# Kernel optimization log

Measured on AMD Instinct MI355X. Metric: run time of the kernel, lower is better.

## Reference

```python
import jax, jax.numpy as jnp
import numpy as np

B, S, H = 2, 2048, 2048
N_HEADS, N_KV, HEAD_DIM = 16, 8, 128
EPS = 1e-6
ROPE_THETA = 1e6


def _rms_norm(x, w, eps=EPS):
    # per-head RMSNorm over last dim (head_dim), computed in fp32
    xf = x.astype(jnp.float32)
    var = jnp.mean(xf * xf, axis=-1, keepdims=True)
    return (w * (xf * jax.lax.rsqrt(var + eps))).astype(x.dtype)


def _rotate_half(x):
    x1, x2 = jnp.split(x, 2, axis=-1)
    return jnp.concatenate((-x2, x1), axis=-1)


def setup_inputs() -> dict:
    key = jax.random.key(0)
    ks = jax.random.split(key, 6)
    hidden_states = jax.random.normal(ks[0], (B, S, H), dtype=jnp.float32)
    # RoPE tables: [B, S, head_dim]
    inv_freq = 1.0 / (ROPE_THETA ** (np.arange(0, HEAD_DIM, 2, dtype=np.float32) / HEAD_DIM))
    pos = np.arange(S, dtype=np.float32)
    freqs = np.outer(pos, inv_freq)                      # [S, head_dim/2]
    emb = np.concatenate([freqs, freqs], axis=-1)        # [S, head_dim]
    cos = jnp.broadcast_to(jnp.asarray(np.cos(emb)), (B, S, HEAD_DIM))
    sin = jnp.broadcast_to(jnp.asarray(np.sin(emb)), (B, S, HEAD_DIM))
    # additive causal mask [B, 1, S, S]
    causal = jnp.triu(jnp.full((S, S), -1e9, dtype=jnp.float32), k=1)
    attention_mask = jnp.broadcast_to(causal[None, None], (B, 1, S, S))
    scale = 0.02
    Wq = jax.random.normal(ks[1], (N_HEADS * HEAD_DIM, H), dtype=jnp.float32) * scale
    Wk = jax.random.normal(ks[2], (N_KV * HEAD_DIM, H), dtype=jnp.float32) * scale
    Wv = jax.random.normal(ks[3], (N_KV * HEAD_DIM, H), dtype=jnp.float32) * scale
    Wo = jax.random.normal(ks[4], (H, N_HEADS * HEAD_DIM), dtype=jnp.float32) * scale
    q_norm_w = jnp.ones((HEAD_DIM,), dtype=jnp.float32)
    k_norm_w = jnp.ones((HEAD_DIM,), dtype=jnp.float32)
    return dict(hidden_states=hidden_states, cos=cos, sin=sin,
                attention_mask=attention_mask, Wq=Wq, Wk=Wk, Wv=Wv, Wo=Wo,
                q_norm_w=q_norm_w, k_norm_w=k_norm_w)


def reference(hidden_states, cos, sin, attention_mask, Wq, Wk, Wv, Wo, q_norm_w, k_norm_w):
    b, s, _ = hidden_states.shape
    scaling = HEAD_DIM ** -0.5
    n_rep = N_HEADS // N_KV
    # QKV projections (torch Linear: x @ W.T), split into heads
    q = jnp.einsum('bsh,dh->bsd', hidden_states, Wq).reshape(b, s, N_HEADS, HEAD_DIM)
    k = jnp.einsum('bsh,dh->bsd', hidden_states, Wk).reshape(b, s, N_KV, HEAD_DIM)
    v = jnp.einsum('bsh,dh->bsd', hidden_states, Wv).reshape(b, s, N_KV, HEAD_DIM)
    # per-head QK RMSNorm, then [B, H, S, D]
    q = _rms_norm(q, q_norm_w).transpose(0, 2, 1, 3)
    k = _rms_norm(k, k_norm_w).transpose(0, 2, 1, 3)
    v = v.transpose(0, 2, 1, 3)
    # RoPE (cos/sin unsqueezed over head dim)
    c = cos[:, None, :, :]
    sn = sin[:, None, :, :]
    q = q * c + _rotate_half(q) * sn
    k = k * c + _rotate_half(k) * sn
    # GQA: repeat kv heads
    k = jnp.repeat(k, n_rep, axis=1)
    v = jnp.repeat(v, n_rep, axis=1)
    # eager attention: materialize full [B, H, S, S] scores
    attn_weights = jnp.einsum('bhqd,bhkd->bhqk', q, k) * scaling + attention_mask
    attn_weights = jax.nn.softmax(attn_weights.astype(jnp.float32), axis=-1).astype(q.dtype)
    attn_output = jnp.einsum('bhqk,bhkd->bhqd', attn_weights, v)
    attn_output = attn_output.transpose(0, 2, 1, 3).reshape(b, s, N_HEADS * HEAD_DIM)
    attn_output = jnp.einsum('bsd,hd->bsh', attn_output, Wo)
    return attn_output, attn_weights
```

## Files before the change

### kernel.cpp

```cpp
#include <hip/hip_runtime.h>
#include <stdint.h>

typedef unsigned short u16;
typedef __attribute__((ext_vector_type(8))) short bf16x8;
typedef __attribute__((ext_vector_type(4))) float f32x4;
typedef __attribute__((ext_vector_type(4))) unsigned short u16x4;
typedef __attribute__((ext_vector_type(8))) unsigned short u16x8;

#define SCALE_LOG2E 0.12751743007633614f

__device__ __forceinline__ u16 f2bf(float x){
  uint32_t u = __float_as_uint(x);
  u += 0x7FFFu + ((u >> 16) & 1u);
  return (u16)(u >> 16);
}
__device__ __forceinline__ float bf2f(u16 h){
  return __uint_as_float(((uint32_t)h) << 16);
}
__device__ __forceinline__ void gload16(const void* g, void* l){
  __builtin_amdgcn_global_load_lds((const __attribute__((address_space(1))) void*)g,
                                   (__attribute__((address_space(3))) void*)l, 16, 0, 0);
}

__global__ __launch_bounds__(256) void k_cvt5(
    const float* __restrict__ s0, u16* __restrict__ d0,
    const float* __restrict__ s1, u16* __restrict__ d1,
    const float* __restrict__ s2, u16* __restrict__ d2,
    const float* __restrict__ s3, u16* __restrict__ d3,
    const float* __restrict__ s4, u16* __restrict__ d4)
{
  int b = blockIdx.x;
  const float* s; u16* d; int off;
  if      (b < 8192)  { s=s0; d=d0; off=b; }
  else if (b < 12288) { s=s1; d=d1; off=b-8192; }
  else if (b < 14336) { s=s2; d=d2; off=b-12288; }
  else if (b < 16384) { s=s3; d=d3; off=b-14336; }
  else                { s=s4; d=d4; off=b-16384; }
  size_t i = ((size_t)off * 256 + threadIdx.x) * 4;
  float4 v = *(const float4*)(s + i);
  ushort4 o;
  o.x = f2bf(v.x); o.y = f2bf(v.y); o.z = f2bf(v.z); o.w = f2bf(v.w);
  *(ushort4*)(d + i) = o;
}

#define STAGE_UNIT(PTR, ROWOFF, BUF, TENS, KS, T1) do{ \
  _Pragma("unroll") \
  for(int jj=0;jj<2;jj++){ \
    int rs_ = wid*32 + jj*16 + (lane>>2); \
    int kp_ = (lane&3) ^ ((rs_>>1)&3); \
    gload16((PTR) + (size_t)((ROWOFF)+rs_)*K + (size_t)(T1)*64 + (KS)*32 + kp_*8, \
            &lds[BUF][TENS][KS][(wid*2+jj)*512]); \
  }}while(0)

#define FRAG(BASE, ROW) (*(const bf16x8*)((BASE) + (ROW)*32 + ((c_ ^ (((ROW)>>1)&3))<<3)))

__global__ __launch_bounds__(512,2) void k_gemm256(
    const u16* __restrict__ A, const u16* __restrict__ Bw, void* __restrict__ Cout,
    int N, int K, int ldc, int out_f32)
{
  __shared__ u16 lds[2][2][2][256*32];
  const int tid = threadIdx.x, wid = tid>>6, lane = tid&63;
  const int nbn = N >> 8;
  const int cpx = gridDim.x >> 3;
  const int bid = (blockIdx.x & 7)*cpx + (blockIdx.x >> 3);
  const int bm = bid / nbn, bn = bid % nbn;
  const int m0 = bm<<8, n0 = bn<<8;
  const int wm = wid>>2, wn = wid&3;
  const int c_ = lane>>4, rl = lane&15;

  f32x4 acc[8][4];
  f32x4 zero4 = {0.f,0.f,0.f,0.f};
#pragma unroll
  for (int i=0;i<8;i++)
#pragma unroll
    for (int j=0;j<4;j++) acc[i][j] = zero4;

  STAGE_UNIT(A,  m0, 0, 0, 0, 0);
  STAGE_UNIT(Bw, n0, 0, 1, 0, 0);
  STAGE_UNIT(A,  m0, 0, 0, 1, 0);
  STAGE_UNIT(Bw, n0, 0, 1, 1, 0);

  const int nt = K >> 6;
#pragma unroll 2
  for (int t=0; t<nt; ++t) {
    const int cur = t&1, nxt = cur^1;
    const bool pf = (t+1 < nt);
    const u16* Ab0 = lds[cur][0][0];
    const u16* Bb0 = lds[cur][1][0];
    const u16* Ab1 = lds[cur][0][1];
    const u16* Bb1 = lds[cur][1][1];
    bf16x8 af[4], bf[4];

    asm volatile("s_waitcnt vmcnt(4)" ::: "memory");
    __builtin_amdgcn_s_barrier();
    asm volatile("" ::: "memory");
#pragma unroll
    for (int j=0;j<4;j++) bf[j] = FRAG(Bb0, wn*64 + j*16 + rl);
#pragma unroll
    for (int i=0;i<4;i++) af[i] = FRAG(Ab0, wm*128 + i*16 + rl);
    if (pf) STAGE_UNIT(A, m0, nxt, 0, 0, t+1);
    __builtin_amdgcn_s_setprio(1);
#pragma unroll
    for (int i=0;i<4;i++)
#pragma unroll
      for (int j=0;j<4;j++)
        acc[i][j] = __builtin_amdgcn_mfma_f32_16x16x32_bf16(af[i], bf[j], acc[i][j], 0,0,0);
    __builtin_amdgcn_s_setprio(0);
    __builtin_amdgcn_s_barrier();
    asm volatile("" ::: "memory");

#pragma unroll
    for (int i=0;i<4;i++) af[i] = FRAG(Ab0, wm*128 + (i+4)*16 + rl);
    if (pf) STAGE_UNIT(Bw, n0, nxt, 1, 0, t+1);
    __builtin_amdgcn_s_setprio(1);
#pragma unroll
    for (int i=0;i<4;i++)
#pragma unroll
      for (int j=0;j<4;j++)
        acc[i+4][j] = __builtin_amdgcn_mfma_f32_16x16x32_bf16(af[i], bf[j], acc[i+4][j], 0,0,0);
    __builtin_amdgcn_s_setprio(0);
    __builtin_amdgcn_s_barrier();
    asm volatile("" ::: "memory");

    if (pf) { asm volatile("s_waitcnt vmcnt(4)" ::: "memory"); }
    else    { asm volatile("s_waitcnt vmcnt(0)" ::: "memory"); }
    __builtin_amdgcn_s_barrier();
    asm volatile("" ::: "memory");
#pragma unroll
    for (int j=0;j<4;j++) bf[j] = FRAG(Bb1, wn*64 + j*16 + rl);
#pragma unroll
    for (int i=0;i<4;i++) af[i] = FRAG(Ab1, wm*128 + i*16 + rl);
    if (pf) STAGE_UNIT(A, m0, nxt, 0, 1, t+1);
    __builtin_amdgcn_s_setprio(1);
#pragma unroll
    for (int i=0;i<4;i++)
#pragma unroll
      for (int j=0;j<4;j++)
        acc[i][j] = __builtin_amdgcn_mfma_f32_16x16x32_bf16(af[i], bf[j], acc[i][j], 0,0,0);
    __builtin_amdgcn_s_setprio(0);
    __builtin_amdgcn_s_barrier();
    asm volatile("" ::: "memory");

#pragma unroll
    for (int i=0;i<4;i++) af[i] = FRAG(Ab1, wm*128 + (i+4)*16 + rl);
    if (pf) STAGE_UNIT(Bw, n0, nxt, 1, 1, t+1);
    __builtin_amdgcn_s_setprio(1);
#pragma unroll
    for (int i=0;i<4;i++)
#pragma unroll
      for (int j=0;j<4;j++)
        acc[i+4][j] = __builtin_amdgcn_mfma_f32_16x16x32_bf16(af[i], bf[j], acc[i+4][j], 0,0,0);
    __builtin_amdgcn_s_setprio(0);
    __builtin_amdgcn_s_barrier();
    asm volatile("" ::: "memory");
  }

  const int r0 = m0 + wm*128 + ((lane>>4)<<2);
  const int c0 = n0 + wn*64 + rl;
  if (out_f32) {
    float* C = (float*)Cout;
#pragma unroll
    for (int i=0;i<8;i++)
#pragma unroll
      for (int j=0;j<4;j++)
#pragma unroll
        for (int r=0;r<4;r++)
          C[(size_t)(r0 + i*16 + r)*ldc + (c0 + j*16)] = acc[i][j][r];
  } else {
    u16* C = (u16*)Cout;
#pragma unroll
    for (int i=0;i<8;i++)
#pragma unroll
      for (int j=0;j<4;j++)
#pragma unroll
        for (int r=0;r<4;r++)
          C[(size_t)(r0 + i*16 + r)*ldc + (c0 + j*16)] = f2bf(acc[i][j][r]);
  }
}

#define STAGE_A128(BUF, KS, T1) do{ \
  int rs_ = wid*16 + (lane>>2); \
  int kp_ = (lane&3) ^ ((rs_>>1)&3); \
  gload16(A + (size_t)(m0+rs_)*K + (size_t)(T1)*64 + (KS)*32 + kp_*8, \
          &ldsA[BUF][KS][wid*512]); \
  }while(0)

#define STAGE_B128(BUF, KS, T1) do{ \
  _Pragma("unroll") \
  for(int jj=0;jj<2;jj++){ \
    int rs_ = wid*32 + jj*16 + (lane>>2); \
    int kp_ = (lane&3) ^ ((rs_>>1)&3); \
    gload16(Bw + (size_t)(n0+rs_)*K + (size_t)(T1)*64 + (KS)*32 + kp_*8, \
            &ldsB[BUF][KS][(wid*2+jj)*512]); \
  }}while(0)

__global__ __launch_bounds__(512,2) void k_gemm_bm128(
    const u16* __restrict__ A, const u16* __restrict__ Bw, float* __restrict__ C,
    int N, int K, int ldc)
{
  __shared__ u16 ldsA[2][2][128*32];
  __shared__ u16 ldsB[2][2][256*32];
  const int tid = threadIdx.x, wid = tid>>6, lane = tid&63;
  const int nbn = N >> 8;
  const int cpx = gridDim.x >> 3;
  const int bid = (blockIdx.x & 7)*cpx + (blockIdx.x >> 3);
  const int bm = bid / nbn, bn = bid % nbn;
  const int m0 = bm<<7, n0 = bn<<8;
  const int wm = wid>>2, wn = wid&3;
  const int c_ = lane>>4, rl = lane&15;

  f32x4 acc[4][4];
  f32x4 zero4 = {0.f,0.f,0.f,0.f};
#pragma unroll
  for (int i=0;i<4;i++)
#pragma unroll
    for (int j=0;j<4;j++) acc[i][j] = zero4;

  STAGE_A128(0, 0, 0);
  STAGE_B128(0, 0, 0);
  STAGE_A128(0, 1, 0);
  STAGE_B128(0, 1, 0);

  const int nt = K >> 6;
#pragma unroll 2
  for (int t=0; t<nt; ++t) {
    const int cur = t&1, nxt = cur^1;
    const bool pf = (t+1 < nt);
    bf16x8 af[4], bf[4];

    asm volatile("s_waitcnt vmcnt(3)" ::: "memory");
    __builtin_amdgcn_s_barrier();
    asm volatile("" ::: "memory");
#pragma unroll
    for (int i=0;i<4;i++) af[i] = FRAG(ldsA[cur][0], wm*64 + i*16 + rl);
#pragma unroll
    for (int j=0;j<4;j++) bf[j] = FRAG(ldsB[cur][0], wn*64 + j*16 + rl);
    if (pf) { STAGE_A128(nxt, 0, t+1); STAGE_B128(nxt, 0, t+1); }
    __builtin_amdgcn_s_setprio(1);
#pragma unroll
    for (int i=0;i<4;i++)
#pragma unroll
      for (int j=0;j<4;j++)
        acc[i][j] = __builtin_amdgcn_mfma_f32_16x16x32_bf16(af[i], bf[j], acc[i][j], 0,0,0);
    __builtin_amdgcn_s_setprio(0);
    __builtin_amdgcn_s_barrier();
    asm volatile("" ::: "memory");

    if (pf) { asm volatile("s_waitcnt vmcnt(3)" ::: "memory"); }
    else    { asm volatile("s_waitcnt vmcnt(0)" ::: "memory"); }
    __builtin_amdgcn_s_barrier();
    asm volatile("" ::: "memory");
#pragma unroll
    for (int i=0;i<4;i++) af[i] = FRAG(ldsA[cur][1], wm*64 + i*16 + rl);
#pragma unroll
    for (int j=0;j<4;j++) bf[j] = FRAG(ldsB[cur][1], wn*64 + j*16 + rl);
    if (pf) { STAGE_A128(nxt, 1, t+1); STAGE_B128(nxt, 1, t+1); }
    __builtin_amdgcn_s_setprio(1);
#pragma unroll
    for (int i=0;i<4;i++)
#pragma unroll
      for (int j=0;j<4;j++)
        acc[i][j] = __builtin_amdgcn_mfma_f32_16x16x32_bf16(af[i], bf[j], acc[i][j], 0,0,0);
    __builtin_amdgcn_s_setprio(0);
    __builtin_amdgcn_s_barrier();
    asm volatile("" ::: "memory");
  }

  const int r0 = m0 + wm*64 + ((lane>>4)<<2);
  const int c0 = n0 + wn*64 + rl;
#pragma unroll
  for (int i=0;i<4;i++)
#pragma unroll
    for (int j=0;j<4;j++)
#pragma unroll
      for (int r=0;r<4;r++)
        C[(size_t)(r0 + i*16 + r)*ldc + (c0 + j*16)] = acc[i][j][r];
}

__global__ __launch_bounds__(256) void k_normrope(
    u16* __restrict__ qkv, const float* __restrict__ cosb, const float* __restrict__ sinb,
    const float* __restrict__ qw, const float* __restrict__ kw)
{
  const int tid = threadIdx.x, lane = tid&63;
  const int task = blockIdx.x*4 + (tid>>6);
  int bs, col; const float* w;
  if (task < 65536) { bs = task >> 4; col = (task & 15)*128; w = qw; }
  else { int t2 = task - 65536; bs = t2 >> 3; col = 2048 + (t2 & 7)*128; w = kw; }
  u16* row = qkv + (size_t)bs*4096 + col;
  float x0 = bf2f(row[lane]), x1 = bf2f(row[lane+64]);
  float ss = x0*x0 + x1*x1;
#pragma unroll
  for (int m=1; m<64; m<<=1) ss += __shfl_xor(ss, m, 64);
  float rn = rsqrtf(ss*(1.0f/128.0f) + 1e-6f);
  const float* cp = cosb + (size_t)bs*128;
  const float* sp = sinb + (size_t)bs*128;
  float q0 = x0*rn*w[lane], q1 = x1*rn*w[lane+64];
  float o0 = q0*cp[lane]    - q1*sp[lane];
  float o1 = q1*cp[lane+64] + q0*sp[lane+64];
  row[lane]    = f2bf(o0);
  row[lane+64] = f2bf(o1);
}

__global__ __launch_bounds__(256) void k_vtrans(const u16* __restrict__ qkv, u16* __restrict__ vt)
{
  const int bid = blockIdx.x;
  const int dt = bid & 1, st = (bid>>1)&31, kvh = (bid>>6)&7, b = bid>>9;
  __shared__ u16 tile[64][72];
  const int tid = threadIdx.x;
  const int rr = tid >> 3, c = (tid & 7) * 8;
  const u16* src = qkv + ((size_t)(b*2048 + st*64))*4096 + 3072 + kvh*128 + dt*64;
#pragma unroll
  for (int p=0;p<2;p++){
    int sl = p*32 + rr;
    u16x8 v = *(const u16x8*)(src + (size_t)sl*4096 + c);
#pragma unroll
    for (int e=0;e<8;e++) tile[sl][c+e] = v[e];
  }
  __syncthreads();
  u16* dst = vt + ((size_t)((b*8+kvh)*128 + dt*64))*2048 + st*64;
#pragma unroll
  for (int p=0;p<2;p++){
    int dl = p*32 + rr;
    u16x8 o;
#pragma unroll
    for (int e=0;e<8;e++) o[e] = tile[c+e][dl];
    *(u16x8*)(dst + (size_t)dl*2048 + c) = o;
  }
}

#define STAGE_K(T, DSTBUF) do { \
  _Pragma("unroll") \
  for (int i_=0;i_<4;i_++){ \
    int r_ = wv*16 + i_*4 + (lane>>4); \
    int cs_ = (lane&15) ^ (r_&7); \
    gload16(Kb + (size_t)((T)*64 + r_)*4096 + cs_*8, (DSTBUF) + (wv*4+i_)*512); \
  } } while(0)

#define STAGE_V(T, DSTBUF) do { \
  _Pragma("unroll") \
  for (int i_=0;i_<4;i_++){ \
    int d_ = wv*32 + i_*8 + (lane>>3); \
    int cs_ = (lane&7) ^ (d_&7); \
    gload16(Vb + (size_t)d_*2048 + (T)*64 + cs_*8, (DSTBUF) + (wv*4+i_)*512); \
  } } while(0)

#define COMPUTE_S16(SACC, KBUF) do { \
  _Pragma("unroll") \
  for (int ks_=0;ks_<4;ks_++){ \
    bf16x8 bfr_[4]; \
    _Pragma("unroll") \
    for (int ns_=0;ns_<4;ns_++){ \
      int n_ = ns_*16 + (lane&15); \
      int sl_ = (ks_*4 + (lane>>4)) ^ (n_&7); \
      bfr_[ns_] = *(const bf16x8*)((KBUF) + n_*128 + sl_*8); \
    } \
    _Pragma("unroll") \
    for (int ns_=0;ns_<4;ns_++) \
      SACC[ns_] = __builtin_amdgcn_mfma_f32_16x16x32_bf16(qf[ks_], bfr_[ns_], SACC[ns_], 0,0,0); \
  } } while(0)

__global__ __launch_bounds__(256) void k_lsum(
    const u16* __restrict__ qkv, float* __restrict__ lsum)
{
  __shared__ u16 lK[2][64*128];
  const int tid = threadIdx.x, wv = tid>>6, lane = tid&63;
  const int rl = lane&15, hi = lane>>4;
  const int bh = blockIdx.x & 31;
  const int h = bh & 15, b = bh >> 4;
  const int seg = blockIdx.x >> 5;
  const int kvh = h>>1;
  const u16* Qb = qkv + (size_t)b*2048*4096 + h*128;
  const u16* Kb = qkv + (size_t)b*2048*4096 + 2048 + kvh*128;
  float* lrow = lsum + (size_t)bh*2048;

  f32x4 zero4 = {0.f,0.f,0.f,0.f};
  int jj[8], kk[8];
#pragma unroll
  for (int i=0;i<8;i++){
    int t = seg*8 + i;
    int j = (int)((sqrtf(8.0f*t + 1.0f) - 1.0f)*0.5f);
    while ((j+1)*(j+2)/2 <= t) j++;
    while (j*(j+1)/2 > t) j--;
    jj[i] = j; kk[i] = t - j*(j+1)/2;
  }

  STAGE_K(kk[0], lK[0]);
  asm volatile("s_waitcnt vmcnt(0)" ::: "memory");
  __builtin_amdgcn_s_barrier();
  asm volatile("" ::: "memory");
#pragma unroll
  for (int i=0;i<8;i++){
    const int j = jj[i], kt = kk[i];
    if (i+1 < 8) STAGE_K(kk[i+1], lK[(i+1)&1]);
    asm volatile("" ::: "memory");
    bf16x8 qf[4];
#pragma unroll
    for (int ks=0;ks<4;ks++)
      qf[ks] = *(const bf16x8*)(Qb + (size_t)(j*64 + wv*16 + rl)*4096 + ks*32 + hi*8);
    f32x4 sacc[4];
#pragma unroll
    for (int ns=0;ns<4;ns++) sacc[ns] = zero4;
    COMPUTE_S16(sacc, lK[i&1]);
    const int rb = j*64 + wv*16 + hi*4;
    float part[4] = {0.f,0.f,0.f,0.f};
    if (kt == j) {
#pragma unroll
      for (int ns=0;ns<4;ns++)
#pragma unroll
        for (int r=0;r<4;r++){
          int rg = rb + r, cg = kt*64 + ns*16 + rl;
          float e = __builtin_exp2f(sacc[ns][r]*SCALE_LOG2E);
          part[r] += (cg <= rg) ? e : 0.f;
        }
    } else {
#pragma unroll
      for (int ns=0;ns<4;ns++)
#pragma unroll
        for (int r=0;r<4;r++)
          part[r] += __builtin_exp2f(sacc[ns][r]*SCALE_LOG2E);
    }
#pragma unroll
    for (int m=1;m<16;m<<=1)
#pragma unroll
      for (int r=0;r<4;r++) part[r] += __shfl_xor(part[r], m, 64);
    if (rl == 0) {
#pragma unroll
      for (int r=0;r<4;r++) atomicAdd(&lrow[rb + r], part[r]);
    }
    if (i+1 < 8) {
      asm volatile("s_waitcnt vmcnt(4)" ::: "memory");
      __builtin_amdgcn_s_barrier();
      asm volatile("" ::: "memory");
    }
  }
}

__global__ __launch_bounds__(256) void k_attn2(
    const u16* __restrict__ qkv, const u16* __restrict__ vt,
    const float* __restrict__ lsum, float* __restrict__ probs, u16* __restrict__ attn_o)
{
  __shared__ u16 lK[2][64*128];
  __shared__ u16 lV[2][128*64];
  __shared__ u16 lP[4][16*64];
  const int tid = threadIdx.x, wv = tid>>6, lane = tid&63;
  const int rl = lane&15, hi = lane>>4;
  const int j = 31 - (blockIdx.x >> 5);
  const int bh = blockIdx.x & 31;
  const int h = bh & 15, b = bh >> 4;
  const int kvh = h>>1;
  const int q0 = j<<6;
  const u16* Qb = qkv + (size_t)b*2048*4096 + h*128;
  const u16* Kb = qkv + (size_t)b*2048*4096 + 2048 + kvh*128;
  const u16* Vb = vt + (size_t)(b*8+kvh)*128*2048;

  f32x4 zero4 = {0.f,0.f,0.f,0.f};

  bf16x8 qf[4];
#pragma unroll
  for (int ks=0;ks<4;ks++)
    qf[ks] = *(const bf16x8*)(Qb + (size_t)(q0 + wv*16 + rl)*4096 + ks*32 + hi*8);

  const int nkt = j + 1;
  const int rb = q0 + wv*16 + hi*4;
  float linv[4];
#pragma unroll
  for (int r=0;r<4;r++) linv[r] = 1.0f / lsum[(size_t)bh*2048 + rb + r];

  f32x4 oacc[8];
#pragma unroll
  for (int nd=0;nd<8;nd++) oacc[nd] = zero4;

  u16* pw = lP[wv];
  float* pb = probs + (size_t)bh*2048*2048;

  int cur = 0;
  STAGE_K(0, lK[0]);
  STAGE_V(0, lV[0]);
  asm volatile("s_waitcnt vmcnt(0)" ::: "memory");
  __builtin_amdgcn_s_barrier();
  asm volatile("" ::: "memory");
  for (int t=0; t<nkt; ++t) {
    const bool pf = (t+1 < nkt);
    if (pf) { STAGE_K(t+1, lK[cur^1]); STAGE_V(t+1, lV[cur^1]); }
    asm volatile("" ::: "memory");
    f32x4 sacc[4];
#pragma unroll
    for (int ns=0;ns<4;ns++) sacc[ns] = zero4;
    COMPUTE_S16(sacc, lK[cur]);
    const int cb = t*64;
    if (t == nkt-1) {
#pragma unroll
      for (int ns=0;ns<4;ns++)
#pragma unroll
        for (int r=0;r<4;r++){
          int rg = rb + r, cg = cb + ns*16 + rl;
          float p = (cg <= rg) ? __builtin_exp2f(sacc[ns][r]*SCALE_LOG2E)*linv[r] : 0.f;
          int ql = hi*4 + r, kl = ns*16 + rl;
          pw[ql*64 + (((kl>>3) ^ (ql&7))<<3) + (kl&7)] = f2bf(p);
        }
    } else {
#pragma unroll
      for (int ns=0;ns<4;ns++)
#pragma unroll
        for (int r=0;r<4;r++){
          float p = __builtin_exp2f(sacc[ns][r]*SCALE_LOG2E)*linv[r];
          int ql = hi*4 + r, kl = ns*16 + rl;
          pw[ql*64 + (((kl>>3) ^ (ql&7))<<3) + (kl&7)] = f2bf(p);
        }
    }
    {
      const int cq = rl, grp = cq>>1, off = (cq&1)*4;
#pragma unroll
      for (int it=0; it<4; ++it){
        int row = it*4 + hi;
        int slot = grp ^ (row&7);
        u16x4 pk4 = *(const u16x4*)(pw + row*64 + slot*8 + off);
        f32x4 pf4;
#pragma unroll
        for (int r=0;r<4;r++) pf4[r] = bf2f(pk4[r]);
        __builtin_nontemporal_store(pf4,
          (f32x4*)(pb + (size_t)(q0 + wv*16 + row)*2048 + t*64 + cq*4));
      }
    }
    const u16* vbuf = lV[cur];
#pragma unroll
    for (int kks=0;kks<2;kks++){
      bf16x8 pa;
      {
        int ql = rl;
        int sl = (kks*4 + hi) ^ (ql&7);
        pa = *(const bf16x8*)(pw + ql*64 + sl*8);
      }
#pragma unroll
      for (int nd=0;nd<8;nd++){
        int d = nd*16 + rl;
        int sl = (kks*4 + hi) ^ (d&7);
        bf16x8 vb = *(const bf16x8*)(vbuf + d*64 + sl*8);
        oacc[nd] = __builtin_amdgcn_mfma_f32_16x16x32_bf16(pa, vb, oacc[nd], 0,0,0);
      }
    }
    if (pf) {
      asm volatile("s_waitcnt vmcnt(4)" ::: "memory");
      __builtin_amdgcn_s_barrier();
      asm volatile("" ::: "memory");
    }
    cur ^= 1;
  }

  const int kend = nkt*64;
  f32x4 z4 = {0.f,0.f,0.f,0.f};
  for (int q = wv*16; q < wv*16+16; ++q){
    float* rp = pb + (size_t)(q0 + q)*2048;
    for (int c = kend + lane*4; c < 2048; c += 256)
      __builtin_nontemporal_store(z4, (f32x4*)(rp + c));
  }

#pragma unroll
  for (int nd=0;nd<8;nd++)
#pragma unroll
    for (int r=0;r<4;r++){
      int rg = rb + r;
      int cg = h*128 + nd*16 + rl;
      attn_o[(size_t)(b*2048 + rg)*2048 + cg] = f2bf(oacc[nd][r]);
    }
}

extern "C" void kernel_launch(void* const* d_in, const int* in_sizes, int n_in,
                              void* d_out, int out_size, void* d_ws, size_t ws_size,
                              hipStream_t stream) {
  (void)in_sizes; (void)n_in; (void)out_size; (void)ws_size;
  const float* hs   = (const float*)d_in[0];
  const float* cosb = (const float*)d_in[1];
  const float* sinb = (const float*)d_in[2];
  const float* Wq   = (const float*)d_in[4];
  const float* Wk   = (const float*)d_in[5];
  const float* Wv   = (const float*)d_in[6];
  const float* Wo   = (const float*)d_in[7];
  const float* qw   = (const float*)d_in[8];
  const float* kw   = (const float*)d_in[9];
  float* out   = (float*)d_out;
  float* probs = out + 8388608;

  char* ws = (char*)d_ws;
  u16* hs_b   = (u16*)(ws);
  u16* attn_o = hs_b;
  u16* W_all  = (u16*)(ws + (16u<<20));
  u16* Wo_b   = (u16*)(ws + (32u<<20));
  u16* qkv    = (u16*)(ws + (40u<<20));
  u16* v_t    = (u16*)(ws + (72u<<20));
  float* lsum = (float*)(ws + (80u<<20));

  hipMemsetAsync(lsum, 0, 65536*sizeof(float), stream);
  k_cvt5<<<20480,256,0,stream>>>(hs, hs_b, Wq, W_all, Wk, W_all + 4194304,
                                 Wv, W_all + 6291456, Wo, Wo_b);

  k_gemm256<<<256,512,0,stream>>>(hs_b, W_all, (void*)qkv, 4096, 2048, 4096, 0);
  k_normrope<<<24576,256,0,stream>>>(qkv, cosb, sinb, qw, kw);
  k_lsum<<<2112,256,0,stream>>>(qkv, lsum);
  k_vtrans<<<1024,256,0,stream>>>(qkv, v_t);
  k_attn2<<<1024,256,0,stream>>>(qkv, v_t, lsum, probs, attn_o);
  k_gemm_bm128<<<256,512,0,stream>>>(attn_o, Wo_b, out, 2048, 2048, 2048);
}
```

Before: 368.4 us.

## Fuse softmax row-sum pass into attention kernel with 128-row query tiles

Removes the separate k_lsum kernel, its atomics and its memset. The attention kernel now runs two passes itself: first over K to accumulate each row's exp-sum in registers, then over K and V to write probabilities and compute P·V. Blocks grow to 512 threads covering 128 query rows with a balanced tile order, so K/V staging is shared across 8 waves. Normalisation is folded into the exponent as a log-sum offset, and probabilities are converted to bf16 by truncation instead of rounding. The cost is recomputing QK^T twice inside one kernel and slightly different rounding of the stored probabilities.

```diff
diff --git a/kernel.cpp b/kernel.cpp
--- a/kernel.cpp
+++ b/kernel.cpp
@@ -13,6 +13,9 @@
   uint32_t u = __float_as_uint(x);
   u += 0x7FFFu + ((u >> 16) & 1u);
   return (u16)(u >> 16);
+}
+__device__ __forceinline__ u16 f2bf_trunc(float x){
+  return (u16)(__float_as_uint(x) >> 16);
 }
 __device__ __forceinline__ float bf2f(u16 h){
   return __uint_as_float(((uint32_t)h) << 16);
@@ -328,20 +331,20 @@
   }
 }
 
-#define STAGE_K(T, DSTBUF) do { \
+#define STAGE_K8(T, DSTBUF) do { \
   _Pragma("unroll") \
-  for (int i_=0;i_<4;i_++){ \
-    int r_ = wv*16 + i_*4 + (lane>>4); \
+  for (int i_=0;i_<2;i_++){ \
+    int r_ = wv*8 + i_*4 + (lane>>4); \
     int cs_ = (lane&15) ^ (r_&7); \
-    gload16(Kb + (size_t)((T)*64 + r_)*4096 + cs_*8, (DSTBUF) + (wv*4+i_)*512); \
+    gload16(Kb + (size_t)((T)*64 + r_)*4096 + cs_*8, (DSTBUF) + (wv*2+i_)*512); \
   } } while(0)
 
-#define STAGE_V(T, DSTBUF) do { \
+#define STAGE_V8(T, DSTBUF) do { \
   _Pragma("unroll") \
-  for (int i_=0;i_<4;i_++){ \
-    int d_ = wv*32 + i_*8 + (lane>>3); \
+  for (int i_=0;i_<2;i_++){ \
+    int d_ = wv*16 + i_*8 + (lane>>3); \
     int cs_ = (lane&7) ^ (d_&7); \
-    gload16(Vb + (size_t)d_*2048 + (T)*64 + cs_*8, (DSTBUF) + (wv*4+i_)*512); \
+    gload16(Vb + (size_t)d_*2048 + (T)*64 + cs_*8, (DSTBUF) + (wv*2+i_)*512); \
   } } while(0)
 
 #define COMPUTE_S16(SACC, KBUF) do { \
@@ -359,96 +362,21 @@
       SACC[ns_] = __builtin_amdgcn_mfma_f32_16x16x32_bf16(qf[ks_], bfr_[ns_], SACC[ns_], 0,0,0); \
   } } while(0)
 
-__global__ __launch_bounds__(256) void k_lsum(
-    const u16* __restrict__ qkv, float* __restrict__ lsum)
+__global__ __launch_bounds__(512,4) void k_attn(
+    const u16* __restrict__ qkv, const u16* __restrict__ vt,
+    float* __restrict__ probs, u16* __restrict__ attn_o)
 {
-  __shared__ u16 lK[2][64*128];
+  __shared__ u16 lKV[4][64*128];
+  __shared__ u16 lP[8][16*64];
   const int tid = threadIdx.x, wv = tid>>6, lane = tid&63;
   const int rl = lane&15, hi = lane>>4;
-  const int bh = blockIdx.x & 31;
-  const int h = bh & 15, b = bh >> 4;
-  const int seg = blockIdx.x >> 5;
-  const int kvh = h>>1;
-  const u16* Qb = qkv + (size_t)b*2048*4096 + h*128;
-  const u16* Kb = qkv + (size_t)b*2048*4096 + 2048 + kvh*128;
-  float* lrow = lsum + (size_t)bh*2048;
-
-  f32x4 zero4 = {0.f,0.f,0.f,0.f};
-  int jj[8], kk[8];
-#pragma unroll
-  for (int i=0;i<8;i++){
-    int t = seg*8 + i;
-    int j = (int)((sqrtf(8.0f*t + 1.0f) - 1.0f)*0.5f);
-    while ((j+1)*(j+2)/2 <= t) j++;
-    while (j*(j+1)/2 > t) j--;
-    jj[i] = j; kk[i] = t - j*(j+1)/2;
-  }
-
-  STAGE_K(kk[0], lK[0]);
-  asm volatile("s_waitcnt vmcnt(0)" ::: "memory");
-  __builtin_amdgcn_s_barrier();
-  asm volatile("" ::: "memory");
-#pragma unroll
-  for (int i=0;i<8;i++){
-    const int j = jj[i], kt = kk[i];
-    if (i+1 < 8) STAGE_K(kk[i+1], lK[(i+1)&1]);
-    asm volatile("" ::: "memory");
-    bf16x8 qf[4];
-#pragma unroll
-    for (int ks=0;ks<4;ks++)
-      qf[ks] = *(const bf16x8*)(Qb + (size_t)(j*64 + wv*16 + rl)*4096 + ks*32 + hi*8);
-    f32x4 sacc[4];
-#pragma unroll
-    for (int ns=0;ns<4;ns++) sacc[ns] = zero4;
-    COMPUTE_S16(sacc, lK[i&1]);
-    const int rb = j*64 + wv*16 + hi*4;
-    float part[4] = {0.f,0.f,0.f,0.f};
-    if (kt == j) {
-#pragma unroll
-      for (int ns=0;ns<4;ns++)
-#pragma unroll
-        for (int r=0;r<4;r++){
-          int rg = rb + r, cg = kt*64 + ns*16 + rl;
-          float e = __builtin_exp2f(sacc[ns][r]*SCALE_LOG2E);
-          part[r] += (cg <= rg) ? e : 0.f;
-        }
-    } else {
-#pragma unroll
-      for (int ns=0;ns<4;ns++)
-#pragma unroll
-        for (int r=0;r<4;r++)
-          part[r] += __builtin_exp2f(sacc[ns][r]*SCALE_LOG2E);
-    }
-#pragma unroll
-    for (int m=1;m<16;m<<=1)
-#pragma unroll
-      for (int r=0;r<4;r++) part[r] += __shfl_xor(part[r], m, 64);
-    if (rl == 0) {
-#pragma unroll
-      for (int r=0;r<4;r++) atomicAdd(&lrow[rb + r], part[r]);
-    }
-    if (i+1 < 8) {
-      asm volatile("s_waitcnt vmcnt(4)" ::: "memory");
-      __builtin_amdgcn_s_barrier();
-      asm volatile("" ::: "memory");
-    }
-  }
-}
-
-__global__ __launch_bounds__(256) void k_attn2(
-    const u16* __restrict__ qkv, const u16* __restrict__ vt,
-    const float* __restrict__ lsum, float* __restrict__ probs, u16* __restrict__ attn_o)
-{
-  __shared__ u16 lK[2][64*128];
-  __shared__ u16 lV[2][128*64];
-  __shared__ u16 lP[4][16*64];
-  const int tid = threadIdx.x, wv = tid>>6, lane = tid&63;
-  const int rl = lane&15, hi = lane>>4;
-  const int j = 31 - (blockIdx.x >> 5);
-  const int bh = blockIdx.x & 31;
+  const int bid = blockIdx.x;
+  const int r9 = bid >> 5;
+  const int qt = (r9 < 8) ? (15 - r9) : (r9 - 8);
+  const int bh = bid & 31;
   const int h = bh & 15, b = bh >> 4;
   const int kvh = h>>1;
-  const int q0 = j<<6;
+  const int q0 = qt<<7;
   const u16* Qb = qkv + (size_t)b*2048*4096 + h*128;
   const u16* Kb = qkv + (size_t)b*2048*4096 + 2048 + kvh*128;
   const u16* Vb = vt + (size_t)(b*8+kvh)*128*2048;
@@ -460,11 +388,52 @@
   for (int ks=0;ks<4;ks++)
     qf[ks] = *(const bf16x8*)(Qb + (size_t)(q0 + wv*16 + rl)*4096 + ks*32 + hi*8);
 
-  const int nkt = j + 1;
+  const int nkt = 2*qt + 2;
+  const int tdiag = 2*qt + (wv>>2);
   const int rb = q0 + wv*16 + hi*4;
-  float linv[4];
-#pragma unroll
-  for (int r=0;r<4;r++) linv[r] = 1.0f / lsum[(size_t)bh*2048 + rb + r];
+  float lsum[4] = {0.f,0.f,0.f,0.f};
+
+  STAGE_K8(0, lKV[0]);
+  STAGE_K8(1, lKV[1]);
+  if (nkt > 2) STAGE_K8(2, lKV[2]);
+  for (int t=0; t<nkt; ++t) {
+    if      (t+2 < nkt) { asm volatile("s_waitcnt vmcnt(4)" ::: "memory"); }
+    else if (t+1 < nkt) { asm volatile("s_waitcnt vmcnt(2)" ::: "memory"); }
+    else                { asm volatile("s_waitcnt vmcnt(0)" ::: "memory"); }
+    __syncthreads();
+    if (t+3 < nkt) STAGE_K8(t+3, lKV[(t+3)&3]);
+    asm volatile("" ::: "memory");
+    if (t <= tdiag) {
+      f32x4 sacc[4];
+#pragma unroll
+      for (int ns=0;ns<4;ns++) sacc[ns] = zero4;
+      COMPUTE_S16(sacc, lKV[t&3]);
+      const int cb = t*64 + rl;
+      if (t == tdiag) {
+#pragma unroll
+        for (int ns=0;ns<4;ns++)
+#pragma unroll
+          for (int r=0;r<4;r++){
+            int rg = rb + r, cg = cb + ns*16;
+            float e = __builtin_exp2f(sacc[ns][r]*SCALE_LOG2E);
+            lsum[r] += (cg <= rg) ? e : 0.f;
+          }
+      } else {
+#pragma unroll
+        for (int ns=0;ns<4;ns++)
+#pragma unroll
+          for (int r=0;r<4;r++)
+            lsum[r] += __builtin_exp2f(sacc[ns][r]*SCALE_LOG2E);
+      }
+    }
+  }
+#pragma unroll
+  for (int m=1;m<16;m<<=1)
+#pragma unroll
+    for (int r=0;r<4;r++) lsum[r] += __shfl_xor(lsum[r], m, 64);
+  float Lr[4];
+#pragma unroll
+  for (int r=0;r<4;r++) Lr[r] = -__log2f(lsum[r]);
 
   f32x4 oacc[8];
 #pragma unroll
@@ -474,80 +443,80 @@
   float* pb = probs + (size_t)bh*2048*2048;
 
   int cur = 0;
-  STAGE_K(0, lK[0]);
-  STAGE_V(0, lV[0]);
+  STAGE_K8(0, lKV[0]);
+  STAGE_V8(0, lKV[2]);
   asm volatile("s_waitcnt vmcnt(0)" ::: "memory");
-  __builtin_amdgcn_s_barrier();
-  asm volatile("" ::: "memory");
+  __syncthreads();
   for (int t=0; t<nkt; ++t) {
     const bool pf = (t+1 < nkt);
-    if (pf) { STAGE_K(t+1, lK[cur^1]); STAGE_V(t+1, lV[cur^1]); }
-    asm volatile("" ::: "memory");
-    f32x4 sacc[4];
-#pragma unroll
-    for (int ns=0;ns<4;ns++) sacc[ns] = zero4;
-    COMPUTE_S16(sacc, lK[cur]);
-    const int cb = t*64;
-    if (t == nkt-1) {
-#pragma unroll
-      for (int ns=0;ns<4;ns++)
-#pragma unroll
-        for (int r=0;r<4;r++){
-          int rg = rb + r, cg = cb + ns*16 + rl;
-          float p = (cg <= rg) ? __builtin_exp2f(sacc[ns][r]*SCALE_LOG2E)*linv[r] : 0.f;
-          int ql = hi*4 + r, kl = ns*16 + rl;
-          pw[ql*64 + (((kl>>3) ^ (ql&7))<<3) + (kl&7)] = f2bf(p);
+    if (pf) { STAGE_K8(t+1, lKV[cur^1]); STAGE_V8(t+1, lKV[2+(cur^1)]); }
+    asm volatile("" ::: "memory");
+    if (t <= tdiag) {
+      f32x4 sacc[4];
+#pragma unroll
+      for (int ns=0;ns<4;ns++) sacc[ns] = zero4;
+      COMPUTE_S16(sacc, lKV[cur]);
+      const int cb = t*64 + rl;
+      if (t == tdiag) {
+#pragma unroll
+        for (int ns=0;ns<4;ns++)
+#pragma unroll
+          for (int r=0;r<4;r++){
+            int rg = rb + r, cg = cb + ns*16;
+            float p = (cg <= rg) ? __builtin_exp2f(fmaf(sacc[ns][r], SCALE_LOG2E, Lr[r])) : 0.f;
+            int ql = hi*4 + r, kl = ns*16 + rl;
+            pw[ql*64 + (((kl>>3) ^ (ql&7))<<3) + (kl&7)] = f2bf_trunc(p);
+          }
+      } else {
+#pragma unroll
+        for (int ns=0;ns<4;ns++)
+#pragma unroll
+          for (int r=0;r<4;r++){
+            float p = __builtin_exp2f(fmaf(sacc[ns][r], SCALE_LOG2E, Lr[r]));
+            int ql = hi*4 + r, kl = ns*16 + rl;
+            pw[ql*64 + (((kl>>3) ^ (ql&7))<<3) + (kl&7)] = f2bf_trunc(p);
+          }
+      }
+      {
+        const int cq = rl, grp = cq>>1, off = (cq&1)*4;
+#pragma unroll
+        for (int it=0; it<4; ++it){
+          int row = it*4 + hi;
+          int slot = grp ^ (row&7);
+          u16x4 pk4 = *(const u16x4*)(pw + row*64 + slot*8 + off);
+          f32x4 pf4;
+#pragma unroll
+          for (int r=0;r<4;r++) pf4[r] = bf2f(pk4[r]);
+          __builtin_nontemporal_store(pf4,
+            (f32x4*)(pb + (size_t)(q0 + wv*16 + row)*2048 + t*64 + cq*4));
         }
-    } else {
-#pragma unroll
-      for (int ns=0;ns<4;ns++)
-#pragma unroll
-        for (int r=0;r<4;r++){
-          float p = __builtin_exp2f(sacc[ns][r]*SCALE_LOG2E)*linv[r];
-          int ql = hi*4 + r, kl = ns*16 + rl;
-          pw[ql*64 + (((kl>>3) ^ (ql&7))<<3) + (kl&7)] = f2bf(p);
+      }
+      const u16* vbuf = lKV[2+cur];
+#pragma unroll
+      for (int kks=0;kks<2;kks++){
+        bf16x8 pa;
+        {
+          int ql = rl;
+          int sl = (kks*4 + hi) ^ (ql&7);
+          pa = *(const bf16x8*)(pw + ql*64 + sl*8);
         }
-    }
-    {
-      const int cq = rl, grp = cq>>1, off = (cq&1)*4;
-#pragma unroll
-      for (int it=0; it<4; ++it){
-        int row = it*4 + hi;
-        int slot = grp ^ (row&7);
-        u16x4 pk4 = *(const u16x4*)(pw + row*64 + slot*8 + off);
-        f32x4 pf4;
-#pragma unroll
-        for (int r=0;r<4;r++) pf4[r] = bf2f(pk4[r]);
-        __builtin_nontemporal_store(pf4,
-          (f32x4*)(pb + (size_t)(q0 + wv*16 + row)*2048 + t*64 + cq*4));
-      }
-    }
-    const u16* vbuf = lV[cur];
-#pragma unroll
-    for (int kks=0;kks<2;kks++){
-      bf16x8 pa;
-      {
-        int ql = rl;
-        int sl = (kks*4 + hi) ^ (ql&7);
-        pa = *(const bf16x8*)(pw + ql*64 + sl*8);
-      }
-#pragma unroll
-      for (int nd=0;nd<8;nd++){
-        int d = nd*16 + rl;
-        int sl = (kks*4 + hi) ^ (d&7);
-        bf16x8 vb = *(const bf16x8*)(vbuf + d*64 + sl*8);
-        oacc[nd] = __builtin_amdgcn_mfma_f32_16x16x32_bf16(pa, vb, oacc[nd], 0,0,0);
+#pragma unroll
+        for (int nd=0;nd<8;nd++){
+          int d = nd*16 + rl;
+          int sl = (kks*4 + hi) ^ (d&7);
+          bf16x8 vb = *(const bf16x8*)(vbuf + d*64 + sl*8);
+          oacc[nd] = __builtin_amdgcn_mfma_f32_16x16x32_bf16(pa, vb, oacc[nd], 0,0,0);
+        }
       }
     }
     if (pf) {
       asm volatile("s_waitcnt vmcnt(4)" ::: "memory");
-      __builtin_amdgcn_s_barrier();
-      asm volatile("" ::: "memory");
+      __syncthreads();
     }
     cur ^= 1;
   }
 
-  const int kend = nkt*64;
+  const int kend = (tdiag+1)*64;
   f32x4 z4 = {0.f,0.f,0.f,0.f};
   for (int q = wv*16; q < wv*16+16; ++q){
     float* rp = pb + (size_t)(q0 + q)*2048;
@@ -588,16 +557,13 @@
   u16* Wo_b   = (u16*)(ws + (32u<<20));
   u16* qkv    = (u16*)(ws + (40u<<20));
   u16* v_t    = (u16*)(ws + (72u<<20));
-  float* lsum = (float*)(ws + (80u<<20));
-
-  hipMemsetAsync(lsum, 0, 65536*sizeof(float), stream);
+
   k_cvt5<<<20480,256,0,stream>>>(hs, hs_b, Wq, W_all, Wk, W_all + 4194304,
                                  Wv, W_all + 6291456, Wo, Wo_b);
 
   k_gemm256<<<256,512,0,stream>>>(hs_b, W_all, (void*)qkv, 4096, 2048, 4096, 0);
   k_normrope<<<24576,256,0,stream>>>(qkv, cosb, sinb, qw, kw);
-  k_lsum<<<2112,256,0,stream>>>(qkv, lsum);
   k_vtrans<<<1024,256,0,stream>>>(qkv, v_t);
-  k_attn2<<<1024,256,0,stream>>>(qkv, v_t, lsum, probs, attn_o);
+  k_attn<<<512,512,0,stream>>>(qkv, v_t, probs, attn_o);
   k_gemm_bm128<<<256,512,0,stream>>>(attn_o, Wo_b, out, 2048, 2048, 2048);
 }
```

Result: faster. 318.3 us (-13.6%).
